# Kernel tuning notes

Hardware: AMD Instinct MI355X
Metric: run time of the kernel (lower is better)

## Reference

```python
import jax, jax.numpy as jnp
import numpy as np

B, T, I, H, FC, O = 256, 4096, 63, 50, 64, 2


def setup_inputs() -> dict:
    key = jax.random.key(0)
    ks = jax.random.split(key, 9)
    s_ih = 1.0 / np.sqrt(H)
    inp = {
        "x": jax.random.normal(ks[0], (B, T, I), dtype=jnp.float32),
        # RNN params (PyTorch layout: W_ih [H, I], W_hh [H, H])
        "W_ih": jax.random.uniform(ks[1], (H, I), jnp.float32, -s_ih, s_ih),
        "b_ih": jax.random.uniform(ks[2], (H,), jnp.float32, -s_ih, s_ih),
        "W_hh": jax.random.uniform(ks[3], (H, H), jnp.float32, -s_ih, s_ih),
        "b_hh": jax.random.uniform(ks[4], (H,), jnp.float32, -s_ih, s_ih),
        # MLP head
        "W1": jax.random.uniform(ks[5], (FC, H), jnp.float32, -1.0 / np.sqrt(H), 1.0 / np.sqrt(H)),
        "b1": jax.random.uniform(ks[6], (FC,), jnp.float32, -1.0 / np.sqrt(H), 1.0 / np.sqrt(H)),
        "W2": jax.random.uniform(ks[7], (O, FC), jnp.float32, -1.0 / np.sqrt(FC), 1.0 / np.sqrt(FC)),
        "b2": jax.random.uniform(ks[8], (O,), jnp.float32, -1.0 / np.sqrt(FC), 1.0 / np.sqrt(FC)),
    }
    return inp


def reference(x, W_ih, b_ih, W_hh, b_hh, W1, b1, W2, b2):
    # Precompute input projection for all timesteps in one GEMM: [B, T, H]
    xz = jnp.einsum("bti,hi->bth", x, W_ih) + b_ih
    h0 = jnp.zeros((x.shape[0], W_hh.shape[0]), x.dtype)

    def step(h, xt):  # h: [B, H], xt: [B, H]
        h_new = jnp.tanh(xt + h @ W_hh.T + b_hh)
        return h_new, None

    # scan over time; only the final hidden state is needed (out[:, -1, :])
    hT, _ = jax.lax.scan(step, h0, jnp.swapaxes(xz, 0, 1))
    out = jax.nn.relu(hT @ W1.T + b1) @ W2.T + b2  # [B, O]
    probs = jax.nn.softmax(out, axis=1)
    return jnp.argmax(probs, axis=1).astype(jnp.float32)  # [B]
```

## Files before the change

### kernel.cpp

```cpp
#include <hip/hip_runtime.h>
#include <cstdint>
#include <cstddef>

#define BB 256
#define TT 4096
#define ID 63
#define HH 50
#define FCD 64

typedef float f32x2 __attribute__((ext_vector_type(2)));

__device__ __forceinline__ uint32_t rl_u32(float v, int lane) {
    return (uint32_t)__builtin_amdgcn_readlane(__float_as_int(v), lane);
}
__device__ __forceinline__ float rl_f(float v, int lane) {
    return __int_as_float(__builtin_amdgcn_readlane(__float_as_int(v), lane));
}

__device__ __forceinline__ f32x2 pk_mul(uint64_t hp, f32x2 w) {
    f32x2 d;
    asm("v_pk_mul_f32 %0, %1, %2" : "=v"(d) : "s"(hp), "v"(w));
    return d;
}
__device__ __forceinline__ void pk_fma(f32x2& acc, uint64_t hp, f32x2 w) {
    asm("v_pk_fma_f32 %0, %1, %2, %0" : "+v"(acc) : "s"(hp), "v"(w));
}
__device__ __forceinline__ void pk_fma_vv(f32x2& acc, f32x2 a, f32x2 b) {
    asm("v_pk_fma_f32 %0, %1, %2, %0" : "+v"(acc) : "v"(a), "v"(b));
}

__device__ __forceinline__ float fast_tanh(float x) {
    float e = __builtin_amdgcn_exp2f(x * 2.88539008177792681472f);
    return 1.0f - 2.0f * __builtin_amdgcn_rcpf(e + 1.0f);
}

__global__ __launch_bounds__(64) void proj_kernel(
    const float* __restrict__ x, const float* __restrict__ W_ih,
    const float* __restrict__ b_ih, const float* __restrict__ b_hh,
    float* __restrict__ z)
{
    __shared__ __align__(16) float xs[64 * ID];
    __shared__ __align__(16) float ws[HH * 64];
    const int lane = threadIdx.x;
    const int64_t row0 = (int64_t)blockIdx.x * 64;

    const float4* __restrict__ xin4 = (const float4*)(x + row0 * ID);
    float4* xs4 = (float4*)xs;
#pragma unroll
    for (int i = lane; i < (64 * ID) / 4; i += 64) xs4[i] = xin4[i];

    if (lane < ID) {
#pragma unroll 2
        for (int r = 0; r < HH; ++r) ws[r * 64 + lane] = W_ih[r * ID + lane];
    }
    if (lane < HH) ws[lane * 64 + ID] = b_ih[lane] + b_hh[lane];
    __syncthreads();

    f32x2 xp[31];
    float x62;
#pragma unroll
    for (int p = 0; p < 31; ++p) {
        xp[p].x = xs[lane * ID + 2 * p];
        xp[p].y = xs[lane * ID + 2 * p + 1];
    }
    x62 = xs[lane * ID + 62];
    __syncthreads();

    float* zs = xs;
#pragma unroll 2
    for (int j = 0; j < HH; ++j) {
        const float4* __restrict__ w4 = (const float4*)(ws + j * 64);
        f32x2 c0 = {0.f, 0.f}, c1 = {0.f, 0.f};
#pragma unroll
        for (int m = 0; m < 15; ++m) {
            float4 q = w4[m];
            f32x2 wlo; wlo.x = q.x; wlo.y = q.y;
            f32x2 whi; whi.x = q.z; whi.y = q.w;
            pk_fma_vv(c0, xp[2 * m + 0], wlo);
            pk_fma_vv(c1, xp[2 * m + 1], whi);
        }
        float4 qt = w4[15];
        f32x2 wlo; wlo.x = qt.x; wlo.y = qt.y;
        pk_fma_vv(c0, xp[30], wlo);
        float s = (c0.x + c1.x) + (c0.y + c1.y) + fmaf(x62, qt.z, qt.w);
        zs[lane * HH + j] = s;
    }
    __syncthreads();

    const float2* zs2 = (const float2*)zs;
    float2* __restrict__ zo2 = (float2*)(z + row0 * HH);
#pragma unroll
    for (int i = lane; i < (64 * HH) / 2; i += 64) zo2[i] = zs2[i];
}

__global__ __launch_bounds__(64) void rnn_kernel(
    const float* __restrict__ z, const float* __restrict__ W_hh,
    const float* __restrict__ W1, const float* __restrict__ b1,
    const float* __restrict__ W2, const float* __restrict__ b2,
    float* __restrict__ out)
{
    const int b = blockIdx.x;
    const int lane = threadIdx.x;
    const int j = (lane < HH) ? lane : (HH - 1);

    f32x2 wpk[25];
#pragma unroll
    for (int k = 0; k < 25; ++k) {
        wpk[k].x = W_hh[j * HH + 2 * k];
        wpk[k].y = W_hh[j * HH + 2 * k + 1];
    }

    const float* __restrict__ base = z + (int64_t)b * TT * HH;
    const int col = j;

    float zp[8], zn[8];
#pragma unroll
    for (int u = 0; u < 8; ++u) zp[u] = base[u * HH + col];
    const float* p = base + 8 * HH;

    float vh = 0.f;
    for (int t0 = 0; t0 < TT; t0 += 8) {
        if (t0 + 8 < TT) {
#pragma unroll
            for (int u = 0; u < 8; ++u) zn[u] = p[u * HH + col];
        }
        p += 8 * HH;
#pragma unroll
        for (int u = 0; u < 8; ++u) {
            uint64_t hp[25];
#pragma unroll
            for (int k = 0; k < 25; ++k) {
                uint32_t lo = rl_u32(vh, 2 * k);
                uint32_t hi = rl_u32(vh, 2 * k + 1);
                hp[k] = (uint64_t)lo | ((uint64_t)hi << 32);
            }
            f32x2 accA = pk_mul(hp[0], wpk[0]);
            f32x2 accB = pk_mul(hp[1], wpk[1]);
#pragma unroll
            for (int k = 2; k < 25; k += 2) pk_fma(accA, hp[k], wpk[k]);
#pragma unroll
            for (int k = 3; k < 25; k += 2) pk_fma(accB, hp[k], wpk[k]);
            f32x2 ab = accA + accB;
            float s = zp[u] + (ab.x + ab.y);
            vh = fast_tanh(s);
        }
#pragma unroll
        for (int u = 0; u < 8; ++u) zp[u] = zn[u];
    }

    float f = b1[lane];
#pragma unroll
    for (int k = 0; k < HH; ++k) f = fmaf(rl_f(vh, k), W1[lane * HH + k], f);
    f = fmaxf(f, 0.f);
    float p0 = f * W2[lane];
    float p1 = f * W2[FCD + lane];
#pragma unroll
    for (int off = 32; off > 0; off >>= 1) {
        p0 += __shfl_down(p0, off, 64);
        p1 += __shfl_down(p1, off, 64);
    }
    if (lane == 0) out[b] = ((p1 + b2[1]) > (p0 + b2[0])) ? 1.0f : 0.0f;
}

__global__ __launch_bounds__(64) void rnn_fused_kernel(
    const float* __restrict__ x, const float* __restrict__ W_ih,
    const float* __restrict__ b_ih, const float* __restrict__ W_hh,
    const float* __restrict__ b_hh, const float* __restrict__ W1,
    const float* __restrict__ b1, const float* __restrict__ W2,
    const float* __restrict__ b2, float* __restrict__ out)
{
    const int b = blockIdx.x;
    const int lane = threadIdx.x;
    const int j = (lane < HH) ? lane : (HH - 1);

    float whh[HH];
#pragma unroll
    for (int k = 0; k < HH; ++k) whh[k] = W_hh[j * HH + k];
    float wih[ID];
#pragma unroll
    for (int i = 0; i < ID; ++i) wih[i] = W_ih[j * ID + i];
    const float bias = b_ih[j] + b_hh[j];

    const float* __restrict__ base = x + (int64_t)b * TT * ID;
    const int col = (lane < ID) ? lane : (ID - 1);

    float zp[8], zn[8];
#pragma unroll
    for (int u = 0; u < 8; ++u) zp[u] = base[u * ID + col];

    float vh = 0.f;
    for (int t0 = 0; t0 < TT; t0 += 8) {
        if (t0 + 8 < TT) {
#pragma unroll
            for (int u = 0; u < 8; ++u) zn[u] = base[(int64_t)(t0 + 8 + u) * ID + col];
        }
#pragma unroll
        for (int u = 0; u < 8; ++u) {
            float a0 = bias, a1 = 0.f, a2 = 0.f, a3 = 0.f;
#pragma unroll
            for (int i = 0; i < 60; i += 4) {
                a0 = fmaf(rl_f(zp[u], i + 0), wih[i + 0], a0);
                a1 = fmaf(rl_f(zp[u], i + 1), wih[i + 1], a1);
                a2 = fmaf(rl_f(zp[u], i + 2), wih[i + 2], a2);
                a3 = fmaf(rl_f(zp[u], i + 3), wih[i + 3], a3);
            }
            a0 = fmaf(rl_f(zp[u], 60), wih[60], a0);
            a1 = fmaf(rl_f(zp[u], 61), wih[61], a1);
            a2 = fmaf(rl_f(zp[u], 62), wih[62], a2);
#pragma unroll
            for (int k = 0; k < 48; k += 4) {
                a0 = fmaf(rl_f(vh, k + 0), whh[k + 0], a0);
                a1 = fmaf(rl_f(vh, k + 1), whh[k + 1], a1);
                a2 = fmaf(rl_f(vh, k + 2), whh[k + 2], a2);
                a3 = fmaf(rl_f(vh, k + 3), whh[k + 3], a3);
            }
            a0 = fmaf(rl_f(vh, 48), whh[48], a0);
            a1 = fmaf(rl_f(vh, 49), whh[49], a1);
            vh = fast_tanh((a0 + a2) + (a1 + a3));
        }
#pragma unroll
        for (int u = 0; u < 8; ++u) zp[u] = zn[u];
    }

    float f = b1[lane];
#pragma unroll
    for (int k = 0; k < HH; ++k) f = fmaf(rl_f(vh, k), W1[lane * HH + k], f);
    f = fmaxf(f, 0.f);
    float p0 = f * W2[lane];
    float p1 = f * W2[FCD + lane];
#pragma unroll
    for (int off = 32; off > 0; off >>= 1) {
        p0 += __shfl_down(p0, off, 64);
        p1 += __shfl_down(p1, off, 64);
    }
    if (lane == 0) out[b] = ((p1 + b2[1]) > (p0 + b2[0])) ? 1.0f : 0.0f;
}

extern "C" void kernel_launch(void* const* d_in, const int* in_sizes, int n_in,
                              void* d_out, int out_size, void* d_ws, size_t ws_size,
                              hipStream_t stream)
{
    const float* x    = (const float*)d_in[0];
    const float* W_ih = (const float*)d_in[1];
    const float* b_ih = (const float*)d_in[2];
    const float* W_hh = (const float*)d_in[3];
    const float* b_hh = (const float*)d_in[4];
    const float* W1   = (const float*)d_in[5];
    const float* b1   = (const float*)d_in[6];
    const float* W2   = (const float*)d_in[7];
    const float* b2   = (const float*)d_in[8];
    float* out = (float*)d_out;

    const size_t zbytes = (size_t)BB * TT * HH * sizeof(float);
    if (ws_size >= zbytes) {
        float* z = (float*)d_ws;
        proj_kernel<<<(BB * TT) / 64, 64, 0, stream>>>(x, W_ih, b_ih, b_hh, z);
        rnn_kernel<<<BB, 64, 0, stream>>>(z, W_hh, W1, b1, W2, b2, out);
    } else {
        rnn_fused_kernel<<<BB, 64, 0, stream>>>(x, W_ih, b_ih, W_hh, b_hh,
                                                W1, b1, W2, b2, out);
    }
}
```

Measured before the change: 1.457 ms.

## Broadcast hidden state via LDS in RNN loop; load W_ih as scalar operands

The recurrent step now writes each lane's hidden value to shared memory and reads it back as float4 broadcasts, replacing 50 v_readlane instructions per step. The packed FMAs then take both operands from VGPRs. The projection kernel drops its LDS staging of W_ih and instead loads uniform weights straight from global memory as 64-bit scalar operands. There is no barrier between the LDS write and the read; this relies on a single-wavefront block. The LDS round trip adds latency on the serial critical path in exchange for fewer readlane instructions.

Result: no change. 1.469 ms (+0.8%).

```diff
diff --git a/kernel.cpp b/kernel.cpp
--- a/kernel.cpp
+++ b/kernel.cpp
@@ -17,13 +17,13 @@
     return __int_as_float(__builtin_amdgcn_readlane(__float_as_int(v), lane));
 }
 
-__device__ __forceinline__ f32x2 pk_mul(uint64_t hp, f32x2 w) {
-    f32x2 d;
-    asm("v_pk_mul_f32 %0, %1, %2" : "=v"(d) : "s"(hp), "v"(w));
-    return d;
-}
 __device__ __forceinline__ void pk_fma(f32x2& acc, uint64_t hp, f32x2 w) {
     asm("v_pk_fma_f32 %0, %1, %2, %0" : "+v"(acc) : "s"(hp), "v"(w));
+}
+__device__ __forceinline__ f32x2 pk_mul_vv(f32x2 a, f32x2 b) {
+    f32x2 d;
+    asm("v_pk_mul_f32 %0, %1, %2" : "=v"(d) : "v"(a), "v"(b));
+    return d;
 }
 __device__ __forceinline__ void pk_fma_vv(f32x2& acc, f32x2 a, f32x2 b) {
     asm("v_pk_fma_f32 %0, %1, %2, %0" : "+v"(acc) : "v"(a), "v"(b));
@@ -40,7 +40,6 @@
     float* __restrict__ z)
 {
     __shared__ __align__(16) float xs[64 * ID];
-    __shared__ __align__(16) float ws[HH * 64];
     const int lane = threadIdx.x;
     const int64_t row0 = (int64_t)blockIdx.x * 64;
 
@@ -48,12 +47,6 @@
     float4* xs4 = (float4*)xs;
 #pragma unroll
     for (int i = lane; i < (64 * ID) / 4; i += 64) xs4[i] = xin4[i];
-
-    if (lane < ID) {
-#pragma unroll 2
-        for (int r = 0; r < HH; ++r) ws[r * 64 + lane] = W_ih[r * ID + lane];
-    }
-    if (lane < HH) ws[lane * 64 + ID] = b_ih[lane] + b_hh[lane];
     __syncthreads();
 
     f32x2 xp[31];
@@ -67,23 +60,25 @@
     __syncthreads();
 
     float* zs = xs;
-#pragma unroll 2
+    const uint32_t* __restrict__ wu = (const uint32_t*)W_ih;
+#pragma unroll 1
     for (int j = 0; j < HH; ++j) {
-        const float4* __restrict__ w4 = (const float4*)(ws + j * 64);
+        const int base = j * ID;
+        uint64_t wq[31];
+#pragma unroll
+        for (int m = 0; m < 31; ++m) {
+            wq[m] = (uint64_t)wu[base + 2 * m] | ((uint64_t)wu[base + 2 * m + 1] << 32);
+        }
+        const float w62 = W_ih[base + 62];
+        const float bias = b_ih[j] + b_hh[j];
         f32x2 c0 = {0.f, 0.f}, c1 = {0.f, 0.f};
 #pragma unroll
-        for (int m = 0; m < 15; ++m) {
-            float4 q = w4[m];
-            f32x2 wlo; wlo.x = q.x; wlo.y = q.y;
-            f32x2 whi; whi.x = q.z; whi.y = q.w;
-            pk_fma_vv(c0, xp[2 * m + 0], wlo);
-            pk_fma_vv(c1, xp[2 * m + 1], whi);
-        }
-        float4 qt = w4[15];
-        f32x2 wlo; wlo.x = qt.x; wlo.y = qt.y;
-        pk_fma_vv(c0, xp[30], wlo);
-        float s = (c0.x + c1.x) + (c0.y + c1.y) + fmaf(x62, qt.z, qt.w);
-        zs[lane * HH + j] = s;
+        for (int m = 0; m < 30; m += 2) {
+            pk_fma(c0, wq[m], xp[m]);
+            pk_fma(c1, wq[m + 1], xp[m + 1]);
+        }
+        pk_fma(c0, wq[30], xp[30]);
+        zs[lane * HH + j] = (c0.x + c1.x) + (c0.y + c1.y) + fmaf(x62, w62, bias);
     }
     __syncthreads();
 
@@ -99,6 +94,7 @@
     const float* __restrict__ W2, const float* __restrict__ b2,
     float* __restrict__ out)
 {
+    __shared__ __align__(16) float hb[64];
     const int b = blockIdx.x;
     const int lane = threadIdx.x;
     const int j = (lane < HH) ? lane : (HH - 1);
@@ -118,6 +114,7 @@
     for (int u = 0; u < 8; ++u) zp[u] = base[u * HH + col];
     const float* p = base + 8 * HH;
 
+    const float4* h4 = (const float4*)hb;
     float vh = 0.f;
     for (int t0 = 0; t0 < TT; t0 += 8) {
         if (t0 + 8 < TT) {
@@ -127,19 +124,22 @@
         p += 8 * HH;
 #pragma unroll
         for (int u = 0; u < 8; ++u) {
-            uint64_t hp[25];
-#pragma unroll
-            for (int k = 0; k < 25; ++k) {
-                uint32_t lo = rl_u32(vh, 2 * k);
-                uint32_t hi = rl_u32(vh, 2 * k + 1);
-                hp[k] = (uint64_t)lo | ((uint64_t)hi << 32);
+            hb[lane] = vh;
+            f32x2 hv[25];
+#pragma unroll
+            for (int m = 0; m < 12; ++m) {
+                float4 q = h4[m];
+                hv[2 * m + 0].x = q.x; hv[2 * m + 0].y = q.y;
+                hv[2 * m + 1].x = q.z; hv[2 * m + 1].y = q.w;
             }
-            f32x2 accA = pk_mul(hp[0], wpk[0]);
-            f32x2 accB = pk_mul(hp[1], wpk[1]);
-#pragma unroll
-            for (int k = 2; k < 25; k += 2) pk_fma(accA, hp[k], wpk[k]);
-#pragma unroll
-            for (int k = 3; k < 25; k += 2) pk_fma(accB, hp[k], wpk[k]);
+            hv[24] = ((const f32x2*)hb)[24];
+
+            f32x2 accA = pk_mul_vv(hv[0], wpk[0]);
+            f32x2 accB = pk_mul_vv(hv[1], wpk[1]);
+#pragma unroll
+            for (int k = 2; k < 25; k += 2) pk_fma_vv(accA, hv[k], wpk[k]);
+#pragma unroll
+            for (int k = 3; k < 25; k += 2) pk_fma_vv(accB, hv[k], wpk[k]);
             f32x2 ab = accA + accB;
             float s = zp[u] + (ab.x + ab.y);
             vh = fast_tanh(s);
```
